# Performance work log

Hardware: AMD Instinct MI355X
Metric: run time of the kernel (lower is better)

## Reference

```python
import jax, jax.numpy as jnp
import numpy as np

NEG_SLOPE = 0.2

def _gat_conv(x, W, att_src, att_dst, bias, src, dst, n_nodes):
    # x: [N, F_in], W: [F_in, F_out], att_*: [F_out], bias: [F_out]
    h = x @ W                                   # [N, F_out]
    a_src = h @ att_src                         # [N]
    a_dst = h @ att_dst                         # [N]
    e = a_src[src] + a_dst[dst]                 # [E]
    e = jnp.where(e > 0, e, NEG_SLOPE * e)      # LeakyReLU
    # segment softmax over incoming edges of each destination node
    m = jax.ops.segment_max(e, dst, num_segments=n_nodes)
    ex = jnp.exp(e - m[dst])
    denom = jax.ops.segment_sum(ex, dst, num_segments=n_nodes)
    alpha = ex / denom[dst]                     # [E]
    msg = alpha[:, None] * h[src]               # [E, F_out]
    out = jax.ops.segment_sum(msg, dst, num_segments=n_nodes)
    return out + bias

def setup_inputs() -> dict:
    key = jax.random.key(0)
    ks = jax.random.split(key, 12)
    N, E, F_in, H, F_out = 50000, 800000, 128, 128, 128
    def glorot(k, shape):
        lim = float(np.sqrt(6.0 / sum(shape))) if len(shape) > 1 else float(np.sqrt(6.0 / shape[0]))
        return jax.random.uniform(k, shape, jnp.float32, -lim, lim)
    return {
        "x": jax.random.normal(ks[0], (N, F_in), jnp.float32),
        "edge_index": jax.random.randint(ks[1], (2, E), 0, N, jnp.int64),
        "W1": glorot(ks[2], (F_in, H)),
        "att_src1": glorot(ks[3], (H,)),
        "att_dst1": glorot(ks[4], (H,)),
        "b1": jnp.zeros((H,), jnp.float32),
        "W2": glorot(ks[5], (H, F_out)),
        "att_src2": glorot(ks[6], (F_out,)),
        "att_dst2": glorot(ks[7], (F_out,)),
        "b2": jnp.zeros((F_out,), jnp.float32),
    }

def reference(x, edge_index, W1, att_src1, att_dst1, b1, W2, att_src2, att_dst2, b2):
    n_nodes = x.shape[0]
    # add self loops (PyG GATConv default)
    loops = jnp.arange(n_nodes, dtype=edge_index.dtype)
    src = jnp.concatenate([edge_index[0], loops])
    dst = jnp.concatenate([edge_index[1], loops])
    h = _gat_conv(x, W1, att_src1, att_dst1, b1, src, dst, n_nodes)
    h = jax.nn.relu(h)
    h = _gat_conv(h, W2, att_src2, att_dst2, b2, src, dst, n_nodes)
    return jax.nn.relu(h)
```

## Files before the change

kernel.cpp:

```cpp
#include <hip/hip_runtime.h>
#include <cstdint>

#define NEG_SLOPE 0.2f
#define F 128

#define BKT_SHIFT 7
#define BKT_SIZE  128
#define NBK_PAD   512
#define CHUNK     4096
#define EPT       8
#define CAP       3072

typedef unsigned short u16;
typedef unsigned int u32;
typedef float float8_t __attribute__((ext_vector_type(8)));
typedef float float4_t __attribute__((ext_vector_type(4)));
typedef short short8_t __attribute__((ext_vector_type(8)));

__device__ inline u16 f2bf(float f) {
    u32 u = __float_as_uint(f);
    u32 r = u + 0x7fffu + ((u >> 16) & 1u);
    return (u16)(r >> 16);
}
__device__ inline float bflo(u32 v) { return __uint_as_float(v << 16); }
__device__ inline float bfhi(u32 v) { return __uint_as_float(v & 0xffff0000u); }

__device__ inline void prep_unit(const float* __restrict__ W, u16* __restrict__ Wt, int u) {
    int frag = u >> 6, lane = u & 63;
    int K0 = frag >> 3, nt = frag & 7;
    int kbase = K0 * 32 + (lane >> 4) * 8;
    int n = nt * 16 + (lane & 15);
    u32 w[4];
    #pragma unroll
    for (int p = 0; p < 4; ++p) {
        u16 e0 = f2bf(W[(size_t)(kbase + 2 * p) * F + n]);
        u16 e1 = f2bf(W[(size_t)(kbase + 2 * p + 1) * F + n]);
        w[p] = (u32)e0 | ((u32)e1 << 16);
    }
    uint4 o; o.x = w[0]; o.y = w[1]; o.z = w[2]; o.w = w[3];
    ((uint4*)Wt)[u] = o;
}

__device__ inline int block_excl_scan_512(int v, int tid, int* wsum) {
    int incl = v;
    #pragma unroll
    for (int o = 1; o < 64; o <<= 1) {
        int u = __shfl_up(incl, o);
        if ((tid & 63) >= o) incl += u;
    }
    if ((tid & 63) == 63) wsum[tid >> 6] = incl;
    __syncthreads();
    int woff = 0;
    #pragma unroll
    for (int w0 = 0; w0 < 7; ++w0) woff += (w0 < (tid >> 6)) ? wsum[w0] : 0;
    return woff + incl - v;
}

__global__ void __launch_bounds__(512) scatter_prep_kernel(const int* __restrict__ ei, int E, int tot,
                                                           int* __restrict__ bucketCursor,
                                                           u32* __restrict__ pairs,
                                                           const float* __restrict__ W1, u16* __restrict__ Wt1,
                                                           const float* __restrict__ W2, u16* __restrict__ Wt2,
                                                           int nScatBlocks) {
    if ((int)blockIdx.x >= nScatBlocks) {
        int pb = blockIdx.x - nScatBlocks;
        int u = (pb & 3) * 512 + threadIdx.x;
        if (pb < 4) prep_unit(W1, Wt1, u);
        else        prep_unit(W2, Wt2, u);
        return;
    }
    __shared__ int hist[NBK_PAD], excl[NBK_PAD], lcur[NBK_PAD], runb[NBK_PAD];
    __shared__ int wsum[8];
    __shared__ u32 stage[CHUNK];
    __shared__ u16 bktid[CHUNK];
    int tid = threadIdx.x;
    hist[tid] = 0;
    __syncthreads();
    int base = blockIdx.x * CHUNK;
    int chunkCnt = min(CHUNK, tot - base);
    int rs[EPT], rd[EPT];
    int w = base + tid * EPT;
    if (w + EPT <= E) {
        int4 s0 = *(const int4*)&ei[w];
        int4 s1 = *(const int4*)&ei[w + 4];
        int4 d0 = *(const int4*)&ei[E + w];
        int4 d1 = *(const int4*)&ei[E + w + 4];
        rs[0] = s0.x; rs[1] = s0.y; rs[2] = s0.z; rs[3] = s0.w;
        rs[4] = s1.x; rs[5] = s1.y; rs[6] = s1.z; rs[7] = s1.w;
        rd[0] = d0.x; rd[1] = d0.y; rd[2] = d0.z; rd[3] = d0.w;
        rd[4] = d1.x; rd[5] = d1.y; rd[6] = d1.z; rd[7] = d1.w;
        #pragma unroll
        for (int i = 0; i < EPT; ++i) atomicAdd(&hist[rd[i] >> BKT_SHIFT], 1);
    } else {
        #pragma unroll
        for (int i = 0; i < EPT; ++i) {
            int e = w + i;
            rd[i] = -1;
            if (e < tot) {
                int s, d;
                if (e < E) { s = ei[e]; d = ei[E + e]; } else { s = e - E; d = s; }
                rs[i] = s; rd[i] = d;
                atomicAdd(&hist[d >> BKT_SHIFT], 1);
            }
        }
    }
    __syncthreads();
    int v = hist[tid];
    int ex = block_excl_scan_512(v, tid, wsum);
    excl[tid] = ex;
    lcur[tid] = ex;
    if (v > 0) runb[tid] = tid * CAP + atomicAdd(&bucketCursor[tid], v);
    __syncthreads();
    #pragma unroll
    for (int i = 0; i < EPT; ++i) {
        if (rd[i] >= 0) {
            int b = rd[i] >> BKT_SHIFT;
            int pos = atomicAdd(&lcur[b], 1);
            stage[pos] = ((u32)rs[i] << BKT_SHIFT) | (u32)(rd[i] & (BKT_SIZE - 1));
            bktid[pos] = (u16)b;
        }
    }
    __syncthreads();
    for (int j = tid; j < chunkCnt; j += 512) {
        int b = (int)bktid[j];
        size_t idx = (size_t)runb[b] + (j - excl[b]);
        if (idx < (size_t)(b + 1) * CAP)
            pairs[idx] = stage[j];
    }
}

__global__ void __launch_bounds__(512) bucket_scan_kernel(const int* __restrict__ bucketCursor,
                                                          int* __restrict__ bucketStart) {
    __shared__ int wsum[8];
    int t = threadIdx.x;
    int v = min(bucketCursor[t], CAP);
    int ex = block_excl_scan_512(v, t, wsum);
    bucketStart[t] = ex;
    if (t == NBK_PAD - 1) bucketStart[NBK_PAD] = ex + v;
}

__device__ void build_body(const u32* __restrict__ pairs, const int* __restrict__ bucketStart,
                           int* __restrict__ row_ptr, int* __restrict__ csr,
                           int N, int tot, int b, char* smem) {
    u32* stage  = (u32*)smem;
    int* sorted = (int*)(smem + CAP * 4);
    int* hist   = (int*)(smem + CAP * 8);
    int* pfx    = (int*)(smem + CAP * 8 + 512);
    int* cur    = (int*)(smem + CAP * 8 + 1024);
    int tid = threadIdx.x;
    size_t srcb = (size_t)b * CAP;
    int dstb = bucketStart[b];
    int cnt = bucketStart[b + 1] - dstb;
    if (tid < BKT_SIZE) hist[tid] = 0;
    __syncthreads();
    for (int j = tid; j < cnt; j += 256) {
        u32 p = pairs[srcb + j];
        stage[j] = p;
        atomicAdd(&hist[p & (BKT_SIZE - 1)], 1);
    }
    __syncthreads();
    if (tid < BKT_SIZE) pfx[tid] = hist[tid];
    __syncthreads();
    for (int o = 1; o < BKT_SIZE; o <<= 1) {
        int u = 0;
        if (tid < BKT_SIZE && tid >= o) u = pfx[tid - o];
        __syncthreads();
        if (tid < BKT_SIZE) pfx[tid] += u;
        __syncthreads();
    }
    if (tid < BKT_SIZE) {
        int ex = pfx[tid] - hist[tid];
        cur[tid] = ex;
        int d = b * BKT_SIZE + tid;
        if (d < N) row_ptr[d] = dstb + ex;
    }
    __syncthreads();
    for (int j = tid; j < cnt; j += 256) {
        u32 p = stage[j];
        int pos = atomicAdd(&cur[p & (BKT_SIZE - 1)], 1);
        sorted[pos] = (int)(p >> BKT_SHIFT);
    }
    __syncthreads();
    for (int j = tid; j < cnt; j += 256) csr[(size_t)dstb + j] = sorted[j];
    if (b == 0 && tid == 0) row_ptr[N] = tot;
}

template<int IN_BF16>
__device__ void gemm_body(const void* __restrict__ in, const u16* __restrict__ Wt,
                          const float* __restrict__ att_s, const float* __restrict__ att_d,
                          u16* __restrict__ h, float* __restrict__ asrc, float* __restrict__ adst,
                          int N, int gblk, u16* wlds) {
    int tid = threadIdx.x;
    {
        const uint4* src = (const uint4*)Wt;
        uint4* dst = (uint4*)wlds;
        #pragma unroll
        for (int i = 0; i < 8; ++i) dst[tid + i * 256] = src[tid + i * 256];
    }
    __syncthreads();
    int wave = tid >> 6, lane = tid & 63;
    int li = lane & 15, grp = lane >> 4;
    int rowBase = (gblk * 4 + wave) * 16;
    if (rowBase >= N) return;
    int row = rowBase + li;
    if (row > N - 1) row = N - 1;

    short8_t b[4];
    if (IN_BF16) {
        const u16* xp = (const u16*)in + (size_t)row * F + grp * 8;
        #pragma unroll
        for (int K0 = 0; K0 < 4; ++K0)
            b[K0] = *(const short8_t*)(xp + K0 * 32);
    } else {
        const float* xp = (const float*)in + (size_t)row * F + grp * 8;
        #pragma unroll
        for (int K0 = 0; K0 < 4; ++K0) {
            float8_t xv = *(const float8_t*)(xp + K0 * 32);
            short8_t t;
            #pragma unroll
            for (int i = 0; i < 8; ++i) t[i] = (short)f2bf(xv[i]);
            b[K0] = t;
        }
    }

    float4_t acc[8];
    #pragma unroll
    for (int nt = 0; nt < 8; ++nt) acc[nt] = (float4_t){0.f, 0.f, 0.f, 0.f};
    #pragma unroll
    for (int nt = 0; nt < 8; ++nt) {
        #pragma unroll
        for (int K0 = 0; K0 < 4; ++K0) {
            short8_t a = *(const short8_t*)&wlds[((K0 * 8 + nt) * 64 + lane) * 8];
            acc[nt] = __builtin_amdgcn_mfma_f32_16x16x32_bf16(a, b[K0], acc[nt], 0, 0, 0);
        }
    }

    u16* hr = h + (size_t)row * F + grp * 4;
    #pragma unroll
    for (int nt = 0; nt < 8; ++nt) {
        u32 lo = (u32)f2bf(acc[nt][0]) | ((u32)f2bf(acc[nt][1]) << 16);
        u32 hi = (u32)f2bf(acc[nt][2]) | ((u32)f2bf(acc[nt][3]) << 16);
        uint2 st; st.x = lo; st.y = hi;
        *(uint2*)(hr + (size_t)nt * 16) = st;
    }

    float rs = 0.f, rd = 0.f;
    #pragma unroll
    for (int nt = 0; nt < 8; ++nt) {
        float4 a4 = *(const float4*)(att_s + nt * 16 + grp * 4);
        float4 d4 = *(const float4*)(att_d + nt * 16 + grp * 4);
        rs += acc[nt][0] * a4.x + acc[nt][1] * a4.y + acc[nt][2] * a4.z + acc[nt][3] * a4.w;
        rd += acc[nt][0] * d4.x + acc[nt][1] * d4.y + acc[nt][2] * d4.z + acc[nt][3] * d4.w;
    }
    rs += __shfl_xor(rs, 16); rs += __shfl_xor(rs, 32);
    rd += __shfl_xor(rd, 16); rd += __shfl_xor(rd, 32);
    if (grp == 0) { asrc[row] = rs; adst[row] = rd; }
}

__global__ void __launch_bounds__(256) build_gemm_kernel(
    const u32* __restrict__ pairs, const int* __restrict__ bucketStart,
    int* __restrict__ row_ptr, int* __restrict__ csr, int N, int tot,
    const float* __restrict__ x, const u16* __restrict__ Wt,
    const float* __restrict__ att_s, const float* __restrict__ att_d,
    u16* __restrict__ h, float* __restrict__ asrc, float* __restrict__ adst, int NBK)
{
    __shared__ __align__(16) char smem[32768];
    if ((int)blockIdx.x < NBK) {
        build_body(pairs, bucketStart, row_ptr, csr, N, tot, blockIdx.x, smem);
    } else {
        gemm_body<0>(x, Wt, att_s, att_d, h, asrc, adst, N, blockIdx.x - NBK, (u16*)smem);
    }
}

template<int U>
__device__ __forceinline__ void gfma(const uint4* __restrict__ h4, int lane, int s, float p, int t,
                                     float (&acc)[8]) {
    int ss[U]; float pp[U]; uint4 vv[U];
    #pragma unroll
    for (int i = 0; i < U; ++i) { ss[i] = __shfl(s, t + i, 16); pp[i] = __shfl(p, t + i, 16); }
    #pragma unroll
    for (int i = 0; i < U; ++i) vv[i] = h4[(size_t)ss[i] * 16 + lane];
    #pragma unroll
    for (int i = 0; i < U; ++i) {
        acc[0] = fmaf(pp[i], bflo(vv[i].x), acc[0]);
        acc[1] = fmaf(pp[i], bfhi(vv[i].x), acc[1]);
        acc[2] = fmaf(pp[i], bflo(vv[i].y), acc[2]);
        acc[3] = fmaf(pp[i], bfhi(vv[i].y), acc[3]);
        acc[4] = fmaf(pp[i], bflo(vv[i].z), acc[4]);
        acc[5] = fmaf(pp[i], bfhi(vv[i].z), acc[5]);
        acc[6] = fmaf(pp[i], bflo(vv[i].w), acc[6]);
        acc[7] = fmaf(pp[i], bfhi(vv[i].w), acc[7]);
    }
}

__device__ __forceinline__ float agg_core(
    const u16* __restrict__ h, const float* __restrict__ asrc, float ad,
    int start, int deg, const int* __restrict__ csr, int lane, float (&acc)[8]) {
    const uint4* h4 = (const uint4*)h;
    float denom = 0.f;
    int c0 = 0;
    int cnt = min(16, deg);
    int s = 0; float a = 0.f;
    if (lane < cnt) { s = csr[start + lane]; a = asrc[s]; }
    for (;;) {
        float p = 0.f;
        if (lane < cnt) {
            float e = a + ad;
            e = (e > 0.f) ? e : NEG_SLOPE * e;
            p = __expf(fminf(e, 70.f));
        }
        denom += p;

        int nc0 = c0 + 16;
        int ncnt = min(16, deg - nc0);
        int s2 = 0; float a2 = 0.f;
        if (nc0 < deg && lane < ncnt) { s2 = csr[start + nc0 + lane]; a2 = asrc[s2]; }

        int t = 0;
        for (; t + 8 <= cnt; t += 8) gfma<8>(h4, lane, s, p, t, acc);
        for (; t + 4 <= cnt; t += 4) gfma<4>(h4, lane, s, p, t, acc);
        for (; t < cnt; ++t)         gfma<1>(h4, lane, s, p, t, acc);

        if (nc0 >= deg) break;
        c0 = nc0; cnt = ncnt; s = s2; a = a2;
    }
    #pragma unroll
    for (int o = 1; o < 16; o <<= 1) denom += __shfl_xor(denom, o);
    return denom;
}

#define OL_STRIDE 136
__global__ void __launch_bounds__(256) agg_gemm_kernel(
    const u16* __restrict__ h, const float* __restrict__ asrc, const float* __restrict__ adst,
    const int* __restrict__ row_ptr, const int* __restrict__ csr,
    const float* __restrict__ bias,
    const u16* __restrict__ Wt2, const float* __restrict__ att_s2, const float* __restrict__ att_d2,
    u16* __restrict__ h2, float* __restrict__ asrc2, float* __restrict__ adst2, int N)
{
    __shared__ u16 out_lds[16 * OL_STRIDE];
    __shared__ float sdots[2][4][16];
    int tid = threadIdx.x;
    int gidBase = blockIdx.x * 16;
    int gid = gidBase + (tid >> 4);
    int lane = tid & 15;

    int start = row_ptr[gid];
    int deg = row_ptr[gid + 1] - start;
    float acc[8] = {0.f, 0.f, 0.f, 0.f, 0.f, 0.f, 0.f, 0.f};
    float denom = agg_core(h, asrc, adst[gid], start, deg, csr, lane, acc);
    float inv = 1.0f / denom;
    const float* bp = bias + lane * 8;
    u32 wpk[4];
    #pragma unroll
    for (int p2 = 0; p2 < 4; ++p2) {
        float v0 = fmaf(acc[2 * p2],     inv, bp[2 * p2]);
        float v1 = fmaf(acc[2 * p2 + 1], inv, bp[2 * p2 + 1]);
        v0 = v0 > 0.f ? v0 : 0.f;
        v1 = v1 > 0.f ? v1 : 0.f;
        wpk[p2] = (u32)f2bf(v0) | ((u32)f2bf(v1) << 16);
    }
    {
        uint4 st; st.x = wpk[0]; st.y = wpk[1]; st.z = wpk[2]; st.w = wpk[3];
        *(uint4*)&out_lds[(tid >> 4) * OL_STRIDE + lane * 8] = st;
    }
    __syncthreads();

    int l = tid & 63, wv = tid >> 6;
    int li = l & 15, grp = l >> 4;
    short8_t b[4];
    #pragma unroll
    for (int K0 = 0; K0 < 4; ++K0)
        b[K0] = *(const short8_t*)&out_lds[li * OL_STRIDE + grp * 8 + K0 * 32];

    float rs = 0.f, rd = 0.f;
    #pragma unroll
    for (int q = 0; q < 2; ++q) {
        int nt = wv * 2 + q;
        float4_t acc2 = (float4_t){0.f, 0.f, 0.f, 0.f};
        #pragma unroll
        for (int K0 = 0; K0 < 4; ++K0) {
            short8_t a = *(const short8_t*)&Wt2[((K0 * 8 + nt) * 64 + l) * 8];
            acc2 = __builtin_amdgcn_mfma_f32_16x16x32_bf16(a, b[K0], acc2, 0, 0, 0);
        }
        int row = gidBase + li;
        u32 lo = (u32)f2bf(acc2[0]) | ((u32)f2bf(acc2[1]) << 16);
        u32 hi = (u32)f2bf(acc2[2]) | ((u32)f2bf(acc2[3]) << 16);
        uint2 st; st.x = lo; st.y = hi;
        *(uint2*)(h2 + (size_t)row * F + nt * 16 + grp * 4) = st;
        float4 a4 = *(const float4*)(att_s2 + nt * 16 + grp * 4);
        float4 d4 = *(const float4*)(att_d2 + nt * 16 + grp * 4);
        rs += acc2[0] * a4.x + acc2[1] * a4.y + acc2[2] * a4.z + acc2[3] * a4.w;
        rd += acc2[0] * d4.x + acc2[1] * d4.y + acc2[2] * d4.z + acc2[3] * d4.w;
    }
    rs += __shfl_xor(rs, 16); rs += __shfl_xor(rs, 32);
    rd += __shfl_xor(rd, 16); rd += __shfl_xor(rd, 32);
    if (grp == 0) { sdots[0][wv][li] = rs; sdots[1][wv][li] = rd; }
    __syncthreads();
    if (tid < 16) {
        float s = sdots[0][0][tid] + sdots[0][1][tid] + sdots[0][2][tid] + sdots[0][3][tid];
        float d = sdots[1][0][tid] + sdots[1][1][tid] + sdots[1][2][tid] + sdots[1][3][tid];
        asrc2[gidBase + tid] = s;
        adst2[gidBase + tid] = d;
    }
}

__global__ void __launch_bounds__(256) aggregate_out_kernel(
    const u16* __restrict__ h, const float* __restrict__ asrc, const float* __restrict__ adst,
    const int* __restrict__ row_ptr, const int* __restrict__ csr,
    const float* __restrict__ bias, float* __restrict__ out, int N)
{
    int gid = blockIdx.x * 16 + (threadIdx.x >> 4);
    if (gid >= N) return;
    int lane = threadIdx.x & 15;
    int start = row_ptr[gid];
    int deg = row_ptr[gid + 1] - start;
    float acc[8] = {0.f, 0.f, 0.f, 0.f, 0.f, 0.f, 0.f, 0.f};
    float denom = agg_core(h, asrc, adst[gid], start, deg, csr, lane, acc);
    float inv = 1.0f / denom;
    const float* bp = bias + lane * 8;
    float r[8];
    #pragma unroll
    for (int j = 0; j < 8; ++j) {
        float v = fmaf(acc[j], inv, bp[j]);
        r[j] = v > 0.f ? v : 0.f;
    }
    float4 o0 = make_float4(r[0], r[1], r[2], r[3]);
    float4 o1 = make_float4(r[4], r[5], r[6], r[7]);
    ((float4*)out)[(size_t)gid * 32 + lane * 2]     = o0;
    ((float4*)out)[(size_t)gid * 32 + lane * 2 + 1] = o1;
}

static inline size_t align_up(size_t v, size_t a) { return (v + a - 1) & ~(a - 1); }

extern "C" void kernel_launch(void* const* d_in, const int* in_sizes, int n_in,
                              void* d_out, int out_size, void* d_ws, size_t ws_size,
                              hipStream_t stream) {
    const float* x   = (const float*)d_in[0];
    const int*   ei  = (const int*)d_in[1];
    const float* W1  = (const float*)d_in[2];
    const float* as1 = (const float*)d_in[3];
    const float* ad1 = (const float*)d_in[4];
    const float* b1  = (const float*)d_in[5];
    const float* W2  = (const float*)d_in[6];
    const float* as2 = (const float*)d_in[7];
    const float* ad2 = (const float*)d_in[8];
    const float* b2  = (const float*)d_in[9];

    int N = in_sizes[0] / F;
    int E = in_sizes[1] / 2;
    int tot = E + N;

    char* ws = (char*)d_ws;
    size_t off = 0;
    #define ALLOC(type, name, count)                                    \
        type* name = (type*)(ws + off);                                  \
        off = align_up(off + (size_t)(count) * sizeof(type), 256);
    ALLOC(u16,   h,       (size_t)N * F);
    ALLOC(u16,   h2,      (size_t)N * F);
    ALLOC(float, asrc,    N);
    ALLOC(float, adst,    N);
    ALLOC(float, asrc2,   N);
    ALLOC(float, adst2,   N);
    ALLOC(int,   row_ptr, N + 4);
    ALLOC(int,   csr,     tot);
    ALLOC(u32,   pairs,   (size_t)NBK_PAD * CAP);
    ALLOC(int,   bucketStart,  NBK_PAD + 1);
    ALLOC(int,   bucketCursor, NBK_PAD);
    ALLOC(u16,   Wt1,     16384);
    ALLOC(u16,   Wt2,     16384);
    #undef ALLOC

    hipMemsetAsync(bucketCursor, 0, NBK_PAD * sizeof(int), stream);

    int NBK = (N + BKT_SIZE - 1) / BKT_SIZE;
    int nchunks = (tot + CHUNK - 1) / CHUNK;
    int ngemm = (N + 63) / 64;
    int nagg  = (N + 15) / 16;

    scatter_prep_kernel<<<nchunks + 8, 512, 0, stream>>>(ei, E, tot, bucketCursor, pairs,
                                                         W1, Wt1, W2, Wt2, nchunks);
    bucket_scan_kernel<<<1, NBK_PAD, 0, stream>>>(bucketCursor, bucketStart);
    build_gemm_kernel<<<NBK + ngemm, 256, 0, stream>>>(pairs, bucketStart, row_ptr, csr, N, tot,
                                                       x, Wt1, as1, ad1, h, asrc, adst, NBK);
    agg_gemm_kernel<<<nagg, 256, 0, stream>>>(h, asrc, adst, row_ptr, csr, b1,
                                              Wt2, as2, ad2, h2, asrc2, adst2, N);
    aggregate_out_kernel<<<nagg, 256, 0, stream>>>(h2, asrc2, adst2, row_ptr, csr, b2,
                                                   (float*)d_out, N);
}
```

Before: 191.8 us.

## Fold bucket scan into build blocks and batch first 32 neighbor gathers

Removes the single-block bucket_scan kernel launch. Each build block instead computes its own bucket offset by reducing the capped cursors of all preceding buckets, which costs some redundant reads. The aggregation core is also restructured: the first two 16-edge chunks load their indices and scores up front and issue up to 16 feature-row gathers at once before the FMAs, to raise memory-level parallelism for typical degrees (about 17 on average). The trade-off is higher register pressure from the 16-entry uint4 buffer, and higher-degree chunks lose the previous prefetch of the next chunk.

```diff
diff --git a/kernel.cpp b/kernel.cpp
--- a/kernel.cpp
+++ b/kernel.cpp
@@ -129,17 +129,7 @@
     }
 }
 
-__global__ void __launch_bounds__(512) bucket_scan_kernel(const int* __restrict__ bucketCursor,
-                                                          int* __restrict__ bucketStart) {
-    __shared__ int wsum[8];
-    int t = threadIdx.x;
-    int v = min(bucketCursor[t], CAP);
-    int ex = block_excl_scan_512(v, t, wsum);
-    bucketStart[t] = ex;
-    if (t == NBK_PAD - 1) bucketStart[NBK_PAD] = ex + v;
-}
-
-__device__ void build_body(const u32* __restrict__ pairs, const int* __restrict__ bucketStart,
+__device__ void build_body(const u32* __restrict__ pairs, const int* __restrict__ bucketCursor,
                            int* __restrict__ row_ptr, int* __restrict__ csr,
                            int N, int tot, int b, char* smem) {
     u32* stage  = (u32*)smem;
@@ -147,12 +137,20 @@
     int* hist   = (int*)(smem + CAP * 8);
     int* pfx    = (int*)(smem + CAP * 8 + 512);
     int* cur    = (int*)(smem + CAP * 8 + 1024);
+    int* red    = (int*)(smem + CAP * 8 + 1536);
     int tid = threadIdx.x;
+
+    int part = 0;
+    for (int i = tid; i < b; i += 256) part += min(bucketCursor[i], CAP);
+    #pragma unroll
+    for (int o = 32; o > 0; o >>= 1) part += __shfl_xor(part, o);
+    if ((tid & 63) == 0) red[tid >> 6] = part;
+    if (tid < BKT_SIZE) hist[tid] = 0;
+    __syncthreads();
+    int dstb = red[0] + red[1] + red[2] + red[3];
+    int cnt = min(bucketCursor[b], CAP);
+
     size_t srcb = (size_t)b * CAP;
-    int dstb = bucketStart[b];
-    int cnt = bucketStart[b + 1] - dstb;
-    if (tid < BKT_SIZE) hist[tid] = 0;
-    __syncthreads();
     for (int j = tid; j < cnt; j += 256) {
         u32 p = pairs[srcb + j];
         stage[j] = p;
@@ -258,7 +256,7 @@
 }
 
 __global__ void __launch_bounds__(256) build_gemm_kernel(
-    const u32* __restrict__ pairs, const int* __restrict__ bucketStart,
+    const u32* __restrict__ pairs, const int* __restrict__ bucketCursor,
     int* __restrict__ row_ptr, int* __restrict__ csr, int N, int tot,
     const float* __restrict__ x, const u16* __restrict__ Wt,
     const float* __restrict__ att_s, const float* __restrict__ att_d,
@@ -266,10 +264,17 @@
 {
     __shared__ __align__(16) char smem[32768];
     if ((int)blockIdx.x < NBK) {
-        build_body(pairs, bucketStart, row_ptr, csr, N, tot, blockIdx.x, smem);
+        build_body(pairs, bucketCursor, row_ptr, csr, N, tot, blockIdx.x, smem);
     } else {
         gemm_body<0>(x, Wt, att_s, att_d, h, asrc, adst, N, blockIdx.x - NBK, (u16*)smem);
     }
+}
+
+__device__ __forceinline__ void rowfma(uint4 v, float pp, float (&acc)[8]) {
+    acc[0] = fmaf(pp, bflo(v.x), acc[0]); acc[1] = fmaf(pp, bfhi(v.x), acc[1]);
+    acc[2] = fmaf(pp, bflo(v.y), acc[2]); acc[3] = fmaf(pp, bfhi(v.y), acc[3]);
+    acc[4] = fmaf(pp, bflo(v.z), acc[4]); acc[5] = fmaf(pp, bfhi(v.z), acc[5]);
+    acc[6] = fmaf(pp, bflo(v.w), acc[6]); acc[7] = fmaf(pp, bfhi(v.w), acc[7]);
 }
 
 template<int U>
@@ -281,49 +286,62 @@
     #pragma unroll
     for (int i = 0; i < U; ++i) vv[i] = h4[(size_t)ss[i] * 16 + lane];
     #pragma unroll
-    for (int i = 0; i < U; ++i) {
-        acc[0] = fmaf(pp[i], bflo(vv[i].x), acc[0]);
-        acc[1] = fmaf(pp[i], bfhi(vv[i].x), acc[1]);
-        acc[2] = fmaf(pp[i], bflo(vv[i].y), acc[2]);
-        acc[3] = fmaf(pp[i], bfhi(vv[i].y), acc[3]);
-        acc[4] = fmaf(pp[i], bflo(vv[i].z), acc[4]);
-        acc[5] = fmaf(pp[i], bfhi(vv[i].z), acc[5]);
-        acc[6] = fmaf(pp[i], bflo(vv[i].w), acc[6]);
-        acc[7] = fmaf(pp[i], bfhi(vv[i].w), acc[7]);
-    }
+    for (int i = 0; i < U; ++i) rowfma(vv[i], pp[i], acc);
 }
 
 __device__ __forceinline__ float agg_core(
     const u16* __restrict__ h, const float* __restrict__ asrc, float ad,
     int start, int deg, const int* __restrict__ csr, int lane, float (&acc)[8]) {
     const uint4* h4 = (const uint4*)h;
-    float denom = 0.f;
-    int c0 = 0;
-    int cnt = min(16, deg);
-    int s = 0; float a = 0.f;
-    if (lane < cnt) { s = csr[start + lane]; a = asrc[s]; }
-    for (;;) {
+    int d1 = min(deg, 16), d2 = min(deg - 16, 16);
+    int s1 = 0, s2 = 0; float a1 = 0.f, a2 = 0.f;
+    if (lane < d1) s1 = csr[start + lane];
+    if (lane < d2) s2 = csr[start + 16 + lane];
+    if (lane < d1) a1 = asrc[s1];
+    if (lane < d2) a2 = asrc[s2];
+    float p1 = 0.f, p2 = 0.f;
+    if (lane < d1) {
+        float e = a1 + ad; e = (e > 0.f) ? e : NEG_SLOPE * e;
+        p1 = __expf(fminf(e, 70.f));
+    }
+    if (lane < d2) {
+        float e = a2 + ad; e = (e > 0.f) ? e : NEG_SLOPE * e;
+        p2 = __expf(fminf(e, 70.f));
+    }
+    float denom = p1 + p2;
+
+    uint4 vv[16];
+    #pragma unroll
+    for (int t = 0; t < 16; ++t)
+        if (t < d1) vv[t] = h4[(size_t)__shfl(s1, t, 16) * 16 + lane];
+    #pragma unroll
+    for (int t = 0; t < 16; ++t)
+        if (t < d1) rowfma(vv[t], __shfl(p1, t, 16), acc);
+    if (d2 > 0) {
+        #pragma unroll
+        for (int t = 0; t < 16; ++t)
+            if (t < d2) vv[t] = h4[(size_t)__shfl(s2, t, 16) * 16 + lane];
+        #pragma unroll
+        for (int t = 0; t < 16; ++t)
+            if (t < d2) rowfma(vv[t], __shfl(p2, t, 16), acc);
+    }
+
+    for (int c0 = 32; c0 < deg; c0 += 16) {
+        int cnt = min(16, deg - c0);
+        int s = 0; float a = 0.f;
+        if (lane < cnt) { s = csr[start + c0 + lane]; a = asrc[s]; }
         float p = 0.f;
         if (lane < cnt) {
-            float e = a + ad;
-            e = (e > 0.f) ? e : NEG_SLOPE * e;
+            float e = a + ad; e = (e > 0.f) ? e : NEG_SLOPE * e;
             p = __expf(fminf(e, 70.f));
         }
         denom += p;
-
-        int nc0 = c0 + 16;
-        int ncnt = min(16, deg - nc0);
-        int s2 = 0; float a2 = 0.f;
-        if (nc0 < deg && lane < ncnt) { s2 = csr[start + nc0 + lane]; a2 = asrc[s2]; }
-
         int t = 0;
         for (; t + 8 <= cnt; t += 8) gfma<8>(h4, lane, s, p, t, acc);
         for (; t + 4 <= cnt; t += 4) gfma<4>(h4, lane, s, p, t, acc);
         for (; t < cnt; ++t)         gfma<1>(h4, lane, s, p, t, acc);
-
-        if (nc0 >= deg) break;
-        c0 = nc0; cnt = ncnt; s = s2; a = a2;
-    }
+    }
+
     #pragma unroll
     for (int o = 1; o < 16; o <<= 1) denom += __shfl_xor(denom, o);
     return denom;
@@ -464,7 +482,6 @@
     ALLOC(int,   row_ptr, N + 4);
     ALLOC(int,   csr,     tot);
     ALLOC(u32,   pairs,   (size_t)NBK_PAD * CAP);
-    ALLOC(int,   bucketStart,  NBK_PAD + 1);
     ALLOC(int,   bucketCursor, NBK_PAD);
     ALLOC(u16,   Wt1,     16384);
     ALLOC(u16,   Wt2,     16384);
@@ -479,8 +496,7 @@
 
     scatter_prep_kernel<<<nchunks + 8, 512, 0, stream>>>(ei, E, tot, bucketCursor, pairs,
                                                          W1, Wt1, W2, Wt2, nchunks);
-    bucket_scan_kernel<<<1, NBK_PAD, 0, stream>>>(bucketCursor, bucketStart);
-    build_gemm_kernel<<<NBK + ngemm, 256, 0, stream>>>(pairs, bucketStart, row_ptr, csr, N, tot,
+    build_gemm_kernel<<<NBK + ngemm, 256, 0, stream>>>(pairs, bucketCursor, row_ptr, csr, N, tot,
                                                        x, Wt1, as1, ad1, h, asrc, adst, NBK);
     agg_gemm_kernel<<<nagg, 256, 0, stream>>>(h, asrc, adst, row_ptr, csr, b1,
                                               Wt2, as2, ad2, h2, asrc2, adst2, N);
```

After: 198.2 us. 3.3% more time.
